# Performance work log

Hardware: AMD Instinct MI355X
Metric: run time of the kernel (lower is better)

Reference implementation:

```python
import jax, jax.numpy as jnp
import numpy as np

THRESHOLD = 0.3

def setup_inputs() -> dict:
    key = jax.random.key(0)
    kx, kw = jax.random.split(key)
    x = jax.random.normal(kx, (4, 2048, 2048), dtype=jnp.float32)
    # std 0.2 so a nontrivial fraction of |w| exceeds threshold 0.3
    kernel = 0.2 * jax.random.normal(kw, (2048, 8192), dtype=jnp.float32)
    return {"x": x, "kernel": kernel}

def ternary_quantize(w, threshold=THRESHOLD):
    return jnp.sign(w) * (jnp.abs(w) > threshold)

def ternary_ste(w, threshold=THRESHOLD):
    # Forward: ternary value; backward: identity (STE)
    return w + jax.lax.stop_gradient(ternary_quantize(w, threshold) - w)

def reference(x, kernel):
    w_ternary = ternary_ste(kernel, THRESHOLD)  # values in {-1, 0, +1}
    return x @ w_ternary  # [B, S, features]
```

## Files before the change

kernel.cpp:

```cpp
#include <hip/hip_runtime.h>
#include <hip/hip_bf16.h>
#include <stdint.h>

typedef __attribute__((ext_vector_type(4))) int i32x4;
typedef __attribute__((ext_vector_type(4))) float f32x4;

#define THRESH 0.3f
#define Mdim 8192
#define Kdim 2048
#define Ndim 8192
#define NT 16
#define NIT 8

__global__ void xq_kernel(const float* __restrict__ x,
                          signed char* __restrict__ xq,
                          float* __restrict__ scales) {
  int row = blockIdx.x;
  int tid = threadIdx.x;
  const float* xr = x + (long)row * Kdim;
  float4 a = ((const float4*)xr)[tid * 2];
  float4 b = ((const float4*)xr)[tid * 2 + 1];
  float m = fmaxf(fmaxf(fmaxf(fabsf(a.x), fabsf(a.y)),
                        fmaxf(fabsf(a.z), fabsf(a.w))),
                  fmaxf(fmaxf(fabsf(b.x), fabsf(b.y)),
                        fmaxf(fabsf(b.z), fabsf(b.w))));
  #pragma unroll
  for (int d = 1; d < 64; d <<= 1) m = fmaxf(m, __shfl_xor(m, d, 64));
  __shared__ float red[4];
  if ((tid & 63) == 0) red[tid >> 6] = m;
  __syncthreads();
  m = fmaxf(fmaxf(red[0], red[1]), fmaxf(red[2], red[3]));
  m = fmaxf(m, 1e-20f);
  float inv = 127.0f / m;
  int q0 = (int)rintf(a.x * inv), q1 = (int)rintf(a.y * inv);
  int q2 = (int)rintf(a.z * inv), q3 = (int)rintf(a.w * inv);
  int q4 = (int)rintf(b.x * inv), q5 = (int)rintf(b.y * inv);
  int q6 = (int)rintf(b.z * inv), q7 = (int)rintf(b.w * inv);
  int lo = (q0 & 0xFF) | ((q1 & 0xFF) << 8) | ((q2 & 0xFF) << 16) |
           ((q3 & 0xFF) << 24);
  int hi = (q4 & 0xFF) | ((q5 & 0xFF) << 8) | ((q6 & 0xFF) << 16) |
           ((q7 & 0xFF) << 24);
  ((int2*)(xq + (long)row * Kdim))[tid] = make_int2(lo, hi);
  if (tid == 0) scales[row] = m / 127.0f;
}

__global__ void tern_tr_kernel(const float* __restrict__ w,
                               signed char* __restrict__ bt) {
  __shared__ signed char tile[32][33];
  int n0 = blockIdx.x * 32, k0 = blockIdx.y * 32;
  int tx = threadIdx.x, ty = threadIdx.y;
  #pragma unroll
  for (int j = 0; j < 4; ++j) {
    int k = k0 + ty + j * 8;
    float v = w[(long)k * Ndim + n0 + tx];
    signed char t = (fabsf(v) > THRESH) ? (v > 0.f ? 1 : -1) : 0;
    tile[ty + j * 8][tx] = t;
  }
  __syncthreads();
  int t = ty * 32 + tx;
  int nl = t >> 3, kq = t & 7;
  int b0 = tile[kq * 4 + 0][nl] & 0xFF;
  int b1 = tile[kq * 4 + 1][nl] & 0xFF;
  int b2 = tile[kq * 4 + 2][nl] & 0xFF;
  int b3 = tile[kq * 4 + 3][nl] & 0xFF;
  int pk = b0 | (b1 << 8) | (b2 << 16) | (b3 << 24);
  *(int*)(bt + (long)(n0 + nl) * Kdim + k0 + kq * 4) = pk;
}

__global__ void __launch_bounds__(512, 1) gemm8_kernel(
    const signed char* __restrict__ A,
    const signed char* __restrict__ Bt,
    const float* __restrict__ scales,
    float* __restrict__ C) {
  __shared__ __align__(128) char lds[163840];

  int bid = blockIdx.x;
  int x = bid & 7;
  int o = bid >> 3;
  int c = o >> 5;
  int w = o & 31;
  int tm = x * 4 + (w >> 3);
  int tn = c * 8 + (w & 7);
  long arow0 = (long)tm * 256;
  long bcol0 = (long)tn * 256;

  int tid = threadIdx.x;
  int lane = tid & 63, wid = tid >> 6;
  int wr = wid >> 2, wc = wid & 3;
  int lr = lane & 15, lk = lane >> 4;

  int x7 = lr & 7;
  int voA[2], voB[2];
  #pragma unroll
  for (int ks = 0; ks < 2; ++ks) {
    int xo = ((ks * 4 + lk) ^ x7) << 4;
    voA[ks] = (wr * 128 + lr) * 128 + xo;
    voB[ks] = (wc * 64 + lr) * 128 + xo;
  }

  int go[2][2];
  #pragma unroll
  for (int h = 0; h < 2; ++h)
    #pragma unroll
    for (int cc = 0; cc < 2; ++cc) {
      int s = cc * 512 + tid;
      int r = h * 128 + (s >> 3);
      int co = (s & 7) ^ (r & 7);
      go[h][cc] = r * Kdim + co * 16;
    }
  const char* baseA = (const char*)A + arow0 * (long)Kdim;
  const char* baseB = (const char*)Bt + bcol0 * (long)Kdim;
  int ldst[2] = {(0 * 512 + wid * 64) * 16, (1 * 512 + wid * 64) * 16};

  auto stage = [&](int u, int which, int h) {
    if (u >= NT) return;
    const char* gb = which ? baseB : baseA;
    int base = (which ? (98304 + (u & 1) * 32768) : ((u % 3) * 32768)) +
               h * 16384;
    int ub = u * 128;
    #pragma unroll
    for (int cc = 0; cc < 2; ++cc) {
      const char* g = gb + (long)(go[h][cc] + ub);
      __builtin_amdgcn_global_load_lds(
          (const __attribute__((address_space(1))) void*)g,
          (__attribute__((address_space(3))) void*)(lds + base + ldst[cc]),
          16, 0, 0);
    }
  };

  i32x4 acc[8][4] = {};
  i32x4 bf[4][2];

  stage(0, 0, 0); stage(0, 0, 1); stage(0, 1, 0); stage(0, 1, 1);
  stage(1, 0, 0); stage(1, 0, 1); stage(1, 1, 0); stage(1, 1, 1);
  asm volatile("s_waitcnt vmcnt(8)" ::: "memory");
  __builtin_amdgcn_s_barrier();

  for (int it = 0; it < NIT; ++it) {
    int t = 2 * it;
    #pragma unroll
    for (int half = 0; half < 2; ++half) {
      int cur = t + half;
      const char* pA0 = lds + (cur % 3) * 32768 + voA[0];
      const char* pA1 = lds + (cur % 3) * 32768 + voA[1];
      const char* pB0 = lds + 98304 + (cur & 1) * 32768 + voB[0];
      const char* pB1 = lds + 98304 + (cur & 1) * 32768 + voB[1];
      int u = cur + 2;
      #pragma unroll
      for (int q = 0; q < 4; ++q) {
        i32x4 af[2][2];
        #pragma unroll
        for (int m = 0; m < 2; ++m) {
          af[m][0] = *(const i32x4*)(pA0 + q * 4096 + m * 2048);
          af[m][1] = *(const i32x4*)(pA1 + q * 4096 + m * 2048);
        }
        if (q == 0) {
          #pragma unroll
          for (int n = 0; n < 4; ++n) {
            bf[n][0] = *(const i32x4*)(pB0 + n * 2048);
            bf[n][1] = *(const i32x4*)(pB1 + n * 2048);
          }
        }
        if (q == 0) stage(u, 0, 0);
        else if (q == 1) stage(u, 0, 1);
        else if (q == 2) stage(u, 1, 0);
        else stage(u, 1, 1);

        if (q == 0) asm volatile("s_waitcnt lgkmcnt(8)" ::: "memory");
        __builtin_amdgcn_s_barrier();
        asm volatile("s_waitcnt lgkmcnt(0)" ::: "memory");
        __builtin_amdgcn_s_setprio(1);
        #pragma unroll
        for (int ks = 0; ks < 2; ++ks)
          #pragma unroll
          for (int m = 0; m < 2; ++m)
            #pragma unroll
            for (int n = 0; n < 4; ++n)
              acc[q * 2 + m][n] = __builtin_amdgcn_mfma_i32_16x16x64_i8(
                  af[m][ks], bf[n][ks], acc[q * 2 + m][n], 0, 0, 0);
        __builtin_amdgcn_s_setprio(0);
        if (q == 3) {
          if (u < NT) asm volatile("s_waitcnt vmcnt(8)" ::: "memory");
          else        asm volatile("s_waitcnt vmcnt(0)" ::: "memory");
        }
        __builtin_amdgcn_s_barrier();
      }
    }
  }

  #pragma unroll
  for (int m = 0; m < 8; ++m) {
    long row0 = arow0 + wr * 128 + m * 16 + lk * 4;
    f32x4 sc = *(const f32x4*)(scales + row0);
    #pragma unroll
    for (int n = 0; n < 4; ++n) {
      long col = bcol0 + wc * 64 + n * 16 + lr;
      #pragma unroll
      for (int r = 0; r < 4; ++r)
        C[(row0 + r) * Ndim + col] = (float)acc[m][n][r] * sc[r];
    }
  }
}

__global__ void fallback_gemm(const float* __restrict__ x,
                              const float* __restrict__ w,
                              float* __restrict__ C) {
  __shared__ float As[16][17];
  __shared__ float Bs[16][17];
  int tx = threadIdx.x, ty = threadIdx.y;
  long row = (long)blockIdx.y * 16 + ty;
  long col = (long)blockIdx.x * 16 + tx;
  float s = 0.f;
  for (int k0 = 0; k0 < Kdim; k0 += 16) {
    As[ty][tx] = x[row * Kdim + k0 + tx];
    float v = w[(long)(k0 + ty) * Ndim + col];
    Bs[ty][tx] = (fabsf(v) > THRESH) ? (v > 0.f ? 1.f : -1.f) : 0.f;
    __syncthreads();
    #pragma unroll
    for (int k = 0; k < 16; ++k) s += As[ty][k] * Bs[k][tx];
    __syncthreads();
  }
  C[row * Ndim + col] = s;
}

extern "C" void kernel_launch(void* const* d_in, const int* in_sizes, int n_in,
                              void* d_out, int out_size, void* d_ws, size_t ws_size,
                              hipStream_t stream) {
  const float* x = (const float*)d_in[0];
  const float* w = (const float*)d_in[1];
  float* out = (float*)d_out;

  size_t abytes = (size_t)Mdim * Kdim;
  size_t bbytes = (size_t)Ndim * Kdim;
  size_t sbytes = (size_t)Mdim * 4;

  if (ws_size >= abytes + bbytes + sbytes) {
    signed char* xq = (signed char*)d_ws;
    signed char* bt = (signed char*)d_ws + abytes;
    float* scales = (float*)((char*)d_ws + abytes + bbytes);
    xq_kernel<<<Mdim, 256, 0, stream>>>(x, xq, scales);
    tern_tr_kernel<<<dim3(Ndim / 32, Kdim / 32), dim3(32, 8), 0, stream>>>(w, bt);
    gemm8_kernel<<<1024, 512, 0, stream>>>(xq, bt, scales, out);
  } else {
    fallback_gemm<<<dim3(Ndim / 16, Mdim / 16), dim3(16, 16), 0, stream>>>(x, w, out);
  }
}
```

Before: 185.4 us.

## Load B fragments directly from global into registers, bypassing LDS staging

The B operand is no longer staged through LDS with async global-to-LDS copies. Each wave now reads its B fragments straight from global memory into registers at the start of every k-step. This halves the LDS footprint and removes the B staging and its lgkm waits; the vmcnt thresholds are adjusted to match. The cost is that the global-load latency for B sits right before the first MFMA with no prefetch, and waves that share columns fetch the same B data twice through the cache.

```diff
diff --git a/kernel.cpp b/kernel.cpp
--- a/kernel.cpp
+++ b/kernel.cpp
@@ -72,7 +72,7 @@
     const signed char* __restrict__ Bt,
     const float* __restrict__ scales,
     float* __restrict__ C) {
-  __shared__ __align__(128) char lds[163840];
+  __shared__ __align__(128) char lds[98304];
 
   int bid = blockIdx.x;
   int x = bid & 7;
@@ -90,13 +90,10 @@
   int lr = lane & 15, lk = lane >> 4;
 
   int x7 = lr & 7;
-  int voA[2], voB[2];
-  #pragma unroll
-  for (int ks = 0; ks < 2; ++ks) {
-    int xo = ((ks * 4 + lk) ^ x7) << 4;
-    voA[ks] = (wr * 128 + lr) * 128 + xo;
-    voB[ks] = (wc * 64 + lr) * 128 + xo;
-  }
+  int voA[2];
+  #pragma unroll
+  for (int ks = 0; ks < 2; ++ks)
+    voA[ks] = (wr * 128 + lr) * 128 + ((((ks * 4 + lk) ^ x7)) << 4);
 
   int go[2][2];
   #pragma unroll
@@ -109,18 +106,17 @@
       go[h][cc] = r * Kdim + co * 16;
     }
   const char* baseA = (const char*)A + arow0 * (long)Kdim;
-  const char* baseB = (const char*)Bt + bcol0 * (long)Kdim;
+  const char* baseBlane =
+      (const char*)Bt + (bcol0 + wc * 64 + lr) * (long)Kdim + lk * 16;
   int ldst[2] = {(0 * 512 + wid * 64) * 16, (1 * 512 + wid * 64) * 16};
 
-  auto stage = [&](int u, int which, int h) {
+  auto stage = [&](int u, int h) {
     if (u >= NT) return;
-    const char* gb = which ? baseB : baseA;
-    int base = (which ? (98304 + (u & 1) * 32768) : ((u % 3) * 32768)) +
-               h * 16384;
+    int base = (u % 3) * 32768 + h * 16384;
     int ub = u * 128;
     #pragma unroll
     for (int cc = 0; cc < 2; ++cc) {
-      const char* g = gb + (long)(go[h][cc] + ub);
+      const char* g = baseA + (long)(go[h][cc] + ub);
       __builtin_amdgcn_global_load_lds(
           (const __attribute__((address_space(1))) void*)g,
           (__attribute__((address_space(3))) void*)(lds + base + ldst[cc]),
@@ -131,9 +127,8 @@
   i32x4 acc[8][4] = {};
   i32x4 bf[4][2];
 
-  stage(0, 0, 0); stage(0, 0, 1); stage(0, 1, 0); stage(0, 1, 1);
-  stage(1, 0, 0); stage(1, 0, 1); stage(1, 1, 0); stage(1, 1, 1);
-  asm volatile("s_waitcnt vmcnt(8)" ::: "memory");
+  stage(0, 0); stage(0, 1); stage(1, 0); stage(1, 1);
+  asm volatile("s_waitcnt vmcnt(4)" ::: "memory");
   __builtin_amdgcn_s_barrier();
 
   for (int it = 0; it < NIT; ++it) {
@@ -143,9 +138,15 @@
       int cur = t + half;
       const char* pA0 = lds + (cur % 3) * 32768 + voA[0];
       const char* pA1 = lds + (cur % 3) * 32768 + voA[1];
-      const char* pB0 = lds + 98304 + (cur & 1) * 32768 + voB[0];
-      const char* pB1 = lds + 98304 + (cur & 1) * 32768 + voB[1];
       int u = cur + 2;
+
+      const char* pB = baseBlane + (long)cur * 128;
+      #pragma unroll
+      for (int n = 0; n < 4; ++n) {
+        bf[n][0] = *(const i32x4*)(pB + n * 16 * Kdim);
+        bf[n][1] = *(const i32x4*)(pB + n * 16 * Kdim + 64);
+      }
+
       #pragma unroll
       for (int q = 0; q < 4; ++q) {
         i32x4 af[2][2];
@@ -154,19 +155,9 @@
           af[m][0] = *(const i32x4*)(pA0 + q * 4096 + m * 2048);
           af[m][1] = *(const i32x4*)(pA1 + q * 4096 + m * 2048);
         }
-        if (q == 0) {
-          #pragma unroll
-          for (int n = 0; n < 4; ++n) {
-            bf[n][0] = *(const i32x4*)(pB0 + n * 2048);
-            bf[n][1] = *(const i32x4*)(pB1 + n * 2048);
-          }
-        }
-        if (q == 0) stage(u, 0, 0);
-        else if (q == 1) stage(u, 0, 1);
-        else if (q == 2) stage(u, 1, 0);
-        else stage(u, 1, 1);
-
-        if (q == 0) asm volatile("s_waitcnt lgkmcnt(8)" ::: "memory");
+        if (q == 0) stage(u, 0);
+        else if (q == 1) stage(u, 1);
+
         __builtin_amdgcn_s_barrier();
         asm volatile("s_waitcnt lgkmcnt(0)" ::: "memory");
         __builtin_amdgcn_s_setprio(1);
@@ -180,7 +171,7 @@
                   af[m][ks], bf[n][ks], acc[q * 2 + m][n], 0, 0, 0);
         __builtin_amdgcn_s_setprio(0);
         if (q == 3) {
-          if (u < NT) asm volatile("s_waitcnt vmcnt(8)" ::: "memory");
+          if (u < NT) asm volatile("s_waitcnt vmcnt(4)" ::: "memory");
           else        asm volatile("s_waitcnt vmcnt(0)" ::: "memory");
         }
         __builtin_amdgcn_s_barrier();
```

After: 293.9 us. 58.5% more time.

## Switch int8 GEMM from 16x16x64 to 32x32x32 MFMA with new LDS swizzle

Applied to the files above, without the earlier changes.

Replaces the 16x16x64 int8 MFMA tiling with 32x32x32 int8 MFMA instructions, so each wave computes its 128x64 sub-tile as a 4x2 grid of 32x32 accumulators. The LDS fragment offsets, the XOR swizzle used by the global-to-LDS loads, and the epilogue row/column mapping are all rewritten to match the new operand layout. The aim is fewer MFMA issues and fewer LDS fragment reads per unit of work. The risk is different LDS bank-conflict behaviour and a changed register footprint from the 16-wide accumulators.

```diff
diff --git a/kernel.cpp b/kernel.cpp
--- a/kernel.cpp
+++ b/kernel.cpp
@@ -3,6 +3,7 @@
 #include <stdint.h>
 
 typedef __attribute__((ext_vector_type(4))) int i32x4;
+typedef __attribute__((ext_vector_type(16))) int i32x16;
 typedef __attribute__((ext_vector_type(4))) float f32x4;
 
 #define THRESH 0.3f
@@ -87,15 +88,15 @@
   int tid = threadIdx.x;
   int lane = tid & 63, wid = tid >> 6;
   int wr = wid >> 2, wc = wid & 3;
-  int lr = lane & 15, lk = lane >> 4;
-
-  int x7 = lr & 7;
-  int voA[2], voB[2];
-  #pragma unroll
-  for (int ks = 0; ks < 2; ++ks) {
-    int xo = ((ks * 4 + lk) ^ x7) << 4;
-    voA[ks] = (wr * 128 + lr) * 128 + xo;
-    voB[ks] = (wc * 64 + lr) * 128 + xo;
+  int lo5 = lane & 31, hi = lane >> 5;
+  int f = lo5 >> 2;
+
+  int voA[4], voB[4];
+  #pragma unroll
+  for (int ks = 0; ks < 4; ++ks) {
+    int xo = ((ks * 2 + hi) ^ f) << 4;
+    voA[ks] = (wr * 128 + lo5) * 128 + xo;
+    voB[ks] = (wc * 64 + lo5) * 128 + xo;
   }
 
   int go[2][2];
@@ -105,7 +106,7 @@
     for (int cc = 0; cc < 2; ++cc) {
       int s = cc * 512 + tid;
       int r = h * 128 + (s >> 3);
-      int co = (s & 7) ^ (r & 7);
+      int co = (s & 7) ^ ((s >> 5) & 7);
       go[h][cc] = r * Kdim + co * 16;
     }
   const char* baseA = (const char*)A + arow0 * (long)Kdim;
@@ -128,8 +129,8 @@
     }
   };
 
-  i32x4 acc[8][4] = {};
-  i32x4 bf[4][2];
+  i32x16 acc[4][2] = {};
+  i32x4 bf[2][4];
 
   stage(0, 0, 0); stage(0, 0, 1); stage(0, 1, 0); stage(0, 1, 1);
   stage(1, 0, 0); stage(1, 0, 1); stage(1, 1, 0); stage(1, 1, 1);
@@ -141,25 +142,21 @@
     #pragma unroll
     for (int half = 0; half < 2; ++half) {
       int cur = t + half;
-      const char* pA0 = lds + (cur % 3) * 32768 + voA[0];
-      const char* pA1 = lds + (cur % 3) * 32768 + voA[1];
-      const char* pB0 = lds + 98304 + (cur & 1) * 32768 + voB[0];
-      const char* pB1 = lds + 98304 + (cur & 1) * 32768 + voB[1];
+      const char* pA = lds + (cur % 3) * 32768;
+      const char* pB = lds + 98304 + (cur & 1) * 32768;
       int u = cur + 2;
       #pragma unroll
       for (int q = 0; q < 4; ++q) {
-        i32x4 af[2][2];
+        i32x4 af[4];
         #pragma unroll
-        for (int m = 0; m < 2; ++m) {
-          af[m][0] = *(const i32x4*)(pA0 + q * 4096 + m * 2048);
-          af[m][1] = *(const i32x4*)(pA1 + q * 4096 + m * 2048);
-        }
+        for (int ks = 0; ks < 4; ++ks)
+          af[ks] = *(const i32x4*)(pA + voA[ks] + q * 4096);
         if (q == 0) {
           #pragma unroll
-          for (int n = 0; n < 4; ++n) {
-            bf[n][0] = *(const i32x4*)(pB0 + n * 2048);
-            bf[n][1] = *(const i32x4*)(pB1 + n * 2048);
-          }
+          for (int n = 0; n < 2; ++n)
+            #pragma unroll
+            for (int ks = 0; ks < 4; ++ks)
+              bf[n][ks] = *(const i32x4*)(pB + voB[ks] + n * 4096);
         }
         if (q == 0) stage(u, 0, 0);
         else if (q == 1) stage(u, 0, 1);
@@ -171,13 +168,11 @@
         asm volatile("s_waitcnt lgkmcnt(0)" ::: "memory");
         __builtin_amdgcn_s_setprio(1);
         #pragma unroll
-        for (int ks = 0; ks < 2; ++ks)
+        for (int ks = 0; ks < 4; ++ks)
           #pragma unroll
-          for (int m = 0; m < 2; ++m)
-            #pragma unroll
-            for (int n = 0; n < 4; ++n)
-              acc[q * 2 + m][n] = __builtin_amdgcn_mfma_i32_16x16x64_i8(
-                  af[m][ks], bf[n][ks], acc[q * 2 + m][n], 0, 0, 0);
+          for (int n = 0; n < 2; ++n)
+            acc[q][n] = __builtin_amdgcn_mfma_i32_32x32x32_i8(
+                af[ks], bf[n][ks], acc[q][n], 0, 0, 0);
         __builtin_amdgcn_s_setprio(0);
         if (q == 3) {
           if (u < NT) asm volatile("s_waitcnt vmcnt(8)" ::: "memory");
@@ -189,15 +184,19 @@
   }
 
   #pragma unroll
-  for (int m = 0; m < 8; ++m) {
-    long row0 = arow0 + wr * 128 + m * 16 + lk * 4;
-    f32x4 sc = *(const f32x4*)(scales + row0);
-    #pragma unroll
-    for (int n = 0; n < 4; ++n) {
-      long col = bcol0 + wc * 64 + n * 16 + lr;
+  for (int m = 0; m < 4; ++m) {
+    #pragma unroll
+    for (int n = 0; n < 2; ++n) {
+      long col = bcol0 + wc * 64 + n * 32 + lo5;
       #pragma unroll
-      for (int r = 0; r < 4; ++r)
-        C[(row0 + r) * Ndim + col] = (float)acc[m][n][r] * sc[r];
+      for (int g = 0; g < 4; ++g) {
+        long rowb = arow0 + wr * 128 + m * 32 + g * 8 + hi * 4;
+        f32x4 sc = *(const f32x4*)(scales + rowb);
+        #pragma unroll
+        for (int e = 0; e < 4; ++e)
+          C[(rowb + e) * Ndim + col] =
+              (float)acc[m][n][g * 4 + e] * sc[e];
+      }
     }
   }
 }
```

Result: slower. 190.5 us (+2.8%).
